# Kernel optimization log

Hardware: AMD Instinct MI355X
Metric: run time of the kernel (lower is better)

Reference implementation:

```python
import jax, jax.numpy as jnp
import numpy as np
import math

N, E, B, T = 100000, 500000, 4096, 12
IN, HID, H = 64, 32, 4
HC = HID * H  # 128
ED = 4


def setup_inputs() -> dict:
    key = jax.random.key(0)
    ks = jax.random.split(key, 40)
    w = lambda k, shape: jax.random.normal(k, shape, jnp.float32) * 0.05
    inp = {
        'x': jax.random.normal(ks[0], (N, IN), jnp.float32),
        'edge_index': jax.random.randint(ks[1], (2, E), 0, N, jnp.int32),
        'edge_attr': jax.random.normal(ks[2], (E, ED), jnp.float32),
        'batch': jnp.sort(jax.random.randint(ks[3], (N,), 0, B, jnp.int32)),
        'r_target': jax.random.randint(ks[4], (B,), 0, T, jnp.int32),
        # layer 1 (in=IN)
        'Wq1': w(ks[5], (IN, HC)), 'bq1': w(ks[6], (HC,)),
        'Wk1': w(ks[7], (IN, HC)), 'bk1': w(ks[8], (HC,)),
        'Wv1': w(ks[9], (IN, HC)), 'bv1': w(ks[10], (HC,)),
        'We1': w(ks[11], (ED, HC)),
        'Ws1': w(ks[12], (IN, HC)), 'bs1': w(ks[13], (HC,)),
        # layers 2 and 3 stacked (in=HC)
        'Wq23': w(ks[14], (2, HC, HC)), 'bq23': w(ks[15], (2, HC)),
        'Wk23': w(ks[16], (2, HC, HC)), 'bk23': w(ks[17], (2, HC)),
        'Wv23': w(ks[18], (2, HC, HC)), 'bv23': w(ks[19], (2, HC)),
        'We23': w(ks[20], (2, ED, HC)),
        'Ws23': w(ks[21], (2, HC, HC)), 'bs23': w(ks[22], (2, HC)),
        # per-task linear heads (out_channels=1)
        'head_W': w(ks[23], (T, HC)), 'head_b': w(ks[24], (T,)),
    }
    return inp


def tconv(x, src, dst, ea, Wq, bq, Wk, bk, Wv, bv, We, Ws, bs):
    """PyG TransformerConv: gather -> per-edge MHA score -> segment softmax -> scatter."""
    q = (x @ Wq + bq).reshape(-1, H, HID)   # [N,H,C]
    k = (x @ Wk + bk).reshape(-1, H, HID)
    v = (x @ Wv + bv).reshape(-1, H, HID)
    e = (ea @ We).reshape(-1, H, HID)       # [E,H,C] (lin_edge has no bias)
    kj = k[src] + e                          # [E,H,C]
    alpha = (q[dst] * kj).sum(-1) / math.sqrt(HID)          # [E,H]
    amax = jax.ops.segment_max(alpha, dst, num_segments=N)  # [N,H]
    alpha = jnp.exp(alpha - amax[dst])
    asum = jax.ops.segment_sum(alpha, dst, num_segments=N)
    alpha = alpha / (asum[dst] + 1e-16)
    msg = (v[src] + e) * alpha[..., None]                   # [E,H,C]
    out = jax.ops.segment_sum(msg, dst, num_segments=N).reshape(N, HC)
    return out + x @ Ws + bs                 # root_weight skip connection


def reference(x, edge_index, edge_attr, batch, r_target,
              Wq1, bq1, Wk1, bk1, Wv1, bv1, We1, Ws1, bs1,
              Wq23, bq23, Wk23, bk23, Wv23, bv23, We23, Ws23, bs23,
              head_W, head_b):
    src, dst = edge_index[0], edge_index[1]
    h = jax.nn.relu(tconv(x, src, dst, edge_attr, Wq1, bq1, Wk1, bk1, Wv1, bv1, We1, Ws1, bs1))
    h = jax.nn.relu(tconv(h, src, dst, edge_attr, Wq23[0], bq23[0], Wk23[0], bk23[0], Wv23[0], bv23[0], We23[0], Ws23[0], bs23[0]))
    h = tconv(h, src, dst, edge_attr, Wq23[1], bq23[1], Wk23[1], bk23[1], Wv23[1], bv23[1], We23[1], Ws23[1], bs23[1])
    # global mean pool per graph
    cnt = jax.ops.segment_sum(jnp.ones((N,), h.dtype), batch, num_segments=B)
    pooled = jax.ops.segment_sum(h, batch, num_segments=B) / jnp.maximum(cnt, 1.0)[:, None]  # [B,HC]
    # dropout p=0.3 is a no-op in eval mode
    # per-task head selected by r_target (out_channels=1, squeezed)
    return (pooled * head_W[r_target]).sum(-1) + head_b[r_target]  # [B]
```

## Files before the change

kernel.cpp:

```cpp
#include <hip/hip_runtime.h>
#include <hip/hip_bf16.h>

#define NN 100000
#define EE 500000
#define BB 4096
#define HC 128
#define SCAN_ELEM 1024
#define NSB ((NN + SCAN_ELEM - 1) / SCAN_ELEM)

typedef __bf16 bf16_t;
typedef bf16_t bf16x8 __attribute__((ext_vector_type(8)));
typedef float f32x4 __attribute__((ext_vector_type(4)));

__device__ __forceinline__ unsigned short f2bf(float f) {
    unsigned u = __builtin_bit_cast(unsigned, f);
    u += 0x7FFFu + ((u >> 16) & 1u);
    return (unsigned short)(u >> 16);
}
__device__ __forceinline__ float bflo(unsigned u) {
    return __builtin_bit_cast(float, u << 16);
}
__device__ __forceinline__ float bfhi(unsigned u) {
    return __builtin_bit_cast(float, u & 0xFFFF0000u);
}

__global__ __launch_bounds__(256) void conv_x(const float* __restrict__ in,
                                              unsigned short* __restrict__ outb,
                                              int total4)
{
    const int g = blockIdx.x * 256 + threadIdx.x;
    if (g >= total4) return;
    const float4 f = *(const float4*)(in + (size_t)g * 4);
    ushort4 u;
    u.x = f2bf(f.x); u.y = f2bf(f.y); u.z = f2bf(f.z); u.w = f2bf(f.w);
    *(ushort4*)(outb + (size_t)g * 4) = u;
}

__global__ __launch_bounds__(256) void prep_w(
    const float* __restrict__ Wq, const float* __restrict__ Wk,
    const float* __restrict__ Wv, const float* __restrict__ Ws,
    unsigned short* __restrict__ Wt, int K)
{
    const int g = blockIdx.x * 256 + threadIdx.x;
    const int per = K * 128;
    if (g >= 4 * per) return;
    const int p = g / per, r = g - p * per;
    const int k = r >> 7, n = r & 127;
    const float* W = p == 0 ? Wq : p == 1 ? Wk : p == 2 ? Wv : Ws;
    Wt[(size_t)p * per + (size_t)n * K + k] = f2bf(W[k * 128 + n]);
}

template<int NKT>
__global__ __launch_bounds__(256) void gemm_mfma(
    const unsigned short* __restrict__ A,
    const unsigned short* __restrict__ Wt,
    const float* __restrict__ bq, const float* __restrict__ bk,
    const float* __restrict__ bv, const float* __restrict__ bs,
    unsigned* __restrict__ Qb, unsigned* __restrict__ Kb,
    unsigned* __restrict__ Vb, float* __restrict__ S)
{
    constexpr int K = NKT * 32;
    const int lane = threadIdx.x & 63;
    const int p = threadIdx.x >> 6;
    const int m = lane & 15, kq = lane >> 4;
    const int rows0 = blockIdx.x * 32;

    const unsigned short* Wp = Wt + (size_t)p * 128 * K;
    const float* bias = p == 0 ? bq : p == 1 ? bk : p == 2 ? bv : bs;

    bf16x8 a[2][NKT];
#pragma unroll
    for (int mt = 0; mt < 2; mt++)
#pragma unroll
        for (int kt = 0; kt < NKT; kt++)
            a[mt][kt] = *(const bf16x8*)(A + (size_t)(rows0 + mt * 16 + m) * K + kt * 32 + kq * 8);

    f32x4 acc[2][8];
#pragma unroll
    for (int mt = 0; mt < 2; mt++)
#pragma unroll
        for (int nt = 0; nt < 8; nt++)
            acc[mt][nt] = (f32x4){0.f, 0.f, 0.f, 0.f};

#pragma unroll
    for (int nt = 0; nt < 8; nt++) {
#pragma unroll
        for (int kt = 0; kt < NKT; kt++) {
            const bf16x8 b = *(const bf16x8*)(Wp + (size_t)(nt * 16 + m) * K + kt * 32 + kq * 8);
            acc[0][nt] = __builtin_amdgcn_mfma_f32_16x16x32_bf16(a[0][kt], b, acc[0][nt], 0, 0, 0);
            acc[1][nt] = __builtin_amdgcn_mfma_f32_16x16x32_bf16(a[1][kt], b, acc[1][nt], 0, 0, 0);
        }
    }

    if (p == 3) {
#pragma unroll
        for (int nt = 0; nt < 8; nt++) {
            const float bi = bias[nt * 16 + m];
#pragma unroll
            for (int mt = 0; mt < 2; mt++) {
                float* o = S + (size_t)(rows0 + mt * 16 + kq * 4) * HC + nt * 16 + m;
#pragma unroll
                for (int r = 0; r < 4; r++) o[r * HC] = acc[mt][nt][r] + bi;
            }
        }
    } else {
        unsigned* out = p == 0 ? Qb : p == 1 ? Kb : Vb;
#pragma unroll
        for (int nt = 0; nt < 8; nt++) {
            const float bi = bias[nt * 16 + m];
#pragma unroll
            for (int mt = 0; mt < 2; mt++) {
#pragma unroll
                for (int r = 0; r < 4; r++) {
                    const float v0 = acc[mt][nt][r] + bi;
                    const float v1 = __shfl_xor(v0, 1);
                    if (!(m & 1)) {
                        const unsigned pk = (unsigned)f2bf(v0) | ((unsigned)f2bf(v1) << 16);
                        out[(size_t)(rows0 + mt * 16 + kq * 4 + r) * 64 + nt * 8 + (m >> 1)] = pk;
                    }
                }
            }
        }
    }
}

__global__ __launch_bounds__(256) void deg_k(const int* __restrict__ ei, int* __restrict__ deg)
{
    const int e = blockIdx.x * 256 + threadIdx.x;
    if (e < EE) atomicAdd(&deg[ei[EE + e]], 1);
}

__global__ __launch_bounds__(256) void scan_part(const int* __restrict__ deg,
                                                 int* __restrict__ bsum)
{
    __shared__ int red[256];
    const int base = blockIdx.x * SCAN_ELEM + threadIdx.x * 4;
    int s = 0;
#pragma unroll
    for (int j = 0; j < 4; j++) { const int i = base + j; if (i < NN) s += deg[i]; }
    red[threadIdx.x] = s;
    __syncthreads();
    for (int st = 128; st > 0; st >>= 1) {
        if (threadIdx.x < st) red[threadIdx.x] += red[threadIdx.x + st];
        __syncthreads();
    }
    if (threadIdx.x == 0) bsum[blockIdx.x] = red[0];
}

__global__ __launch_bounds__(128) void scan_top(const int* __restrict__ bsum,
                                                int* __restrict__ boff)
{
    __shared__ int buf[128];
    const int v = (threadIdx.x < NSB) ? bsum[threadIdx.x] : 0;
    buf[threadIdx.x] = v;
    __syncthreads();
    for (int s = 1; s < 128; s <<= 1) {
        const int t = (threadIdx.x >= s) ? buf[threadIdx.x - s] : 0;
        __syncthreads();
        buf[threadIdx.x] += t;
        __syncthreads();
    }
    if (threadIdx.x < NSB) boff[threadIdx.x] = buf[threadIdx.x] - v;
}

__global__ __launch_bounds__(256) void scan_final(const int* __restrict__ deg,
                                                  const int* __restrict__ boff,
                                                  int* __restrict__ off,
                                                  int* __restrict__ cursor)
{
    __shared__ int tsum[256];
    const int base = blockIdx.x * SCAN_ELEM + threadIdx.x * 4;
    int vals[4];
    int s = 0;
#pragma unroll
    for (int j = 0; j < 4; j++) {
        const int i = base + j;
        vals[j] = (i < NN) ? deg[i] : 0;
        s += vals[j];
    }
    tsum[threadIdx.x] = s;
    __syncthreads();
    for (int st = 1; st < 256; st <<= 1) {
        const int t = (threadIdx.x >= st) ? tsum[threadIdx.x - st] : 0;
        __syncthreads();
        tsum[threadIdx.x] += t;
        __syncthreads();
    }
    int ex = boff[blockIdx.x] + tsum[threadIdx.x] - s;
#pragma unroll
    for (int j = 0; j < 4; j++) {
        const int i = base + j;
        if (i < NN) { off[i] = ex; cursor[i] = ex; }
        ex += vals[j];
    }
    if (blockIdx.x == NSB - 1 && threadIdx.x == 255)
        off[NN] = boff[blockIdx.x] + tsum[255];
}

__global__ __launch_bounds__(256) void bucket_k(const int* __restrict__ ei,
                                                const float* __restrict__ ea,
                                                int* __restrict__ cursor,
                                                int* __restrict__ esrc,
                                                float4* __restrict__ eaf)
{
    const int e = blockIdx.x * 256 + threadIdx.x;
    if (e < EE) {
        const int d = ei[EE + e];
        const int p = atomicAdd(&cursor[d], 1);
        esrc[p] = ei[e];
        eaf[p] = *(const float4*)(ea + (size_t)e * 4);
    }
}

__global__ __launch_bounds__(256) void cnt_k(const int* __restrict__ batch,
                                             float* __restrict__ cnt)
{
    const int n = blockIdx.x * 256 + threadIdx.x;
    if (n < NN) atomicAdd(&cnt[batch[n]], 1.0f);
}

__global__ __launch_bounds__(256) void edge_fused(
    const int* __restrict__ esrc, const float4* __restrict__ eaf,
    const float* __restrict__ We,
    const unsigned* __restrict__ Qb, const unsigned* __restrict__ Kb,
    const unsigned* __restrict__ Vb,
    const int* __restrict__ off, const float* __restrict__ S,
    unsigned short* __restrict__ Hb,
    const int* __restrict__ batch, float* __restrict__ pooled,
    int fuse_pool)
{
    const int lane = threadIdx.x & 63;
    const int slot = lane >> 4;
    const int c8   = lane & 15;
    const int n = blockIdx.x * 4 + (threadIdx.x >> 6);

    float w[4][8];
#pragma unroll
    for (int d = 0; d < 4; d++) {
        const float4 a = *(const float4*)(We + d * HC + c8 * 8);
        const float4 b = *(const float4*)(We + d * HC + c8 * 8 + 4);
        w[d][0] = a.x; w[d][1] = a.y; w[d][2] = a.z; w[d][3] = a.w;
        w[d][4] = b.x; w[d][5] = b.y; w[d][6] = b.z; w[d][7] = b.w;
    }

    const uint4 qv = *(const uint4*)(Qb + (size_t)n * 64 + c8 * 4);
    float q[8];
    q[0] = bflo(qv.x); q[1] = bfhi(qv.x); q[2] = bflo(qv.y); q[3] = bfhi(qv.y);
    q[4] = bflo(qv.z); q[5] = bfhi(qv.z); q[6] = bflo(qv.w); q[7] = bfhi(qv.w);

    const int beg = off[n], end = off[n + 1];
    float num[8] = {0.f, 0.f, 0.f, 0.f, 0.f, 0.f, 0.f, 0.f};
    float den = 0.f;

    if (beg < end) {
        int p0 = beg + slot; if (p0 >= end) p0 = end - 1;
        int src = esrc[p0];
        float4 a4 = eaf[p0];
        for (int base = beg; base < end; base += 4) {
            const bool act = (base + slot) < end;
            const uint4 ku = *(const uint4*)(Kb + (size_t)src * 64 + c8 * 4);
            const uint4 vu = *(const uint4*)(Vb + (size_t)src * 64 + c8 * 4);
            const float4 ac = a4;
            if (base + 4 < end) {
                int pn = base + 4 + slot; if (pn >= end) pn = end - 1;
                src = esrc[pn];
                a4 = eaf[pn];
            }
            float e[8];
#pragma unroll
            for (int j = 0; j < 8; j++)
                e[j] = ac.x * w[0][j] + ac.y * w[1][j] + ac.z * w[2][j] + ac.w * w[3][j];
            float part = q[0] * (bflo(ku.x) + e[0]) + q[1] * (bfhi(ku.x) + e[1])
                       + q[2] * (bflo(ku.y) + e[2]) + q[3] * (bfhi(ku.y) + e[3])
                       + q[4] * (bflo(ku.z) + e[4]) + q[5] * (bfhi(ku.z) + e[5])
                       + q[6] * (bflo(ku.w) + e[6]) + q[7] * (bfhi(ku.w) + e[7]);
            part += __shfl_xor(part, 1);
            part += __shfl_xor(part, 2);
            float al = __expf(part * 0.17677669529663687f);
            if (!act) al = 0.f;
            num[0] += (bflo(vu.x) + e[0]) * al;
            num[1] += (bfhi(vu.x) + e[1]) * al;
            num[2] += (bflo(vu.y) + e[2]) * al;
            num[3] += (bfhi(vu.y) + e[3]) * al;
            num[4] += (bflo(vu.z) + e[4]) * al;
            num[5] += (bfhi(vu.z) + e[5]) * al;
            num[6] += (bflo(vu.w) + e[6]) * al;
            num[7] += (bfhi(vu.w) + e[7]) * al;
            den += al;
        }
    }

#pragma unroll
    for (int j = 0; j < 8; j++) {
        num[j] += __shfl_xor(num[j], 16);
        num[j] += __shfl_xor(num[j], 32);
    }
    den += __shfl_xor(den, 16);
    den += __shfl_xor(den, 32);
    const float inv = 1.f / (den + 1e-16f);

    if (!fuse_pool) {
        if (slot == 0) {
            const float4 s0 = *(const float4*)(S + (size_t)n * HC + c8 * 8);
            const float4 s1 = *(const float4*)(S + (size_t)n * HC + c8 * 8 + 4);
            float o[8];
            o[0] = fmaxf(num[0] * inv + s0.x, 0.f);
            o[1] = fmaxf(num[1] * inv + s0.y, 0.f);
            o[2] = fmaxf(num[2] * inv + s0.z, 0.f);
            o[3] = fmaxf(num[3] * inv + s0.w, 0.f);
            o[4] = fmaxf(num[4] * inv + s1.x, 0.f);
            o[5] = fmaxf(num[5] * inv + s1.y, 0.f);
            o[6] = fmaxf(num[6] * inv + s1.z, 0.f);
            o[7] = fmaxf(num[7] * inv + s1.w, 0.f);
            uint4 pk;
            pk.x = (unsigned)f2bf(o[0]) | ((unsigned)f2bf(o[1]) << 16);
            pk.y = (unsigned)f2bf(o[2]) | ((unsigned)f2bf(o[3]) << 16);
            pk.z = (unsigned)f2bf(o[4]) | ((unsigned)f2bf(o[5]) << 16);
            pk.w = (unsigned)f2bf(o[6]) | ((unsigned)f2bf(o[7]) << 16);
            *(uint4*)(Hb + (size_t)n * HC + c8 * 8) = pk;
        }
    } else {
        float oe, oo;
        if      (slot == 0) { oe = num[0]; oo = num[1]; }
        else if (slot == 1) { oe = num[2]; oo = num[3]; }
        else if (slot == 2) { oe = num[4]; oo = num[5]; }
        else                { oe = num[6]; oo = num[7]; }
        const int c = c8 * 8 + slot * 2;
        const float2 s2 = *(const float2*)(S + (size_t)n * HC + c);
        const int b = batch[n];
        atomicAdd(pooled + (size_t)b * HC + c,     oe * inv + s2.x);
        atomicAdd(pooled + (size_t)b * HC + c + 1, oo * inv + s2.y);
    }
}

__global__ __launch_bounds__(256) void head_k(
    const float* __restrict__ pooled, const float* __restrict__ cnt,
    const int* __restrict__ rt, const float* __restrict__ hW,
    const float* __restrict__ hb, float* __restrict__ out)
{
    const int lane = threadIdx.x & 63;
    const int b = blockIdx.x * 4 + (threadIdx.x >> 6);
    if (b >= BB) return;
    const int t = rt[b];
    const int c = lane * 2;
    const float2 p2 = *(const float2*)(pooled + (size_t)b * HC + c);
    const float2 w2 = *(const float2*)(hW + (size_t)t * HC + c);
    float part = p2.x * w2.x + p2.y * w2.y;
    part += __shfl_xor(part, 1);
    part += __shfl_xor(part, 2);
    part += __shfl_xor(part, 4);
    part += __shfl_xor(part, 8);
    part += __shfl_xor(part, 16);
    part += __shfl_xor(part, 32);
    if (lane == 0) out[b] = part / fmaxf(cnt[b], 1.0f) + hb[t];
}

extern "C" void kernel_launch(void* const* d_in, const int* in_sizes, int n_in,
                              void* d_out, int out_size, void* d_ws, size_t ws_size,
                              hipStream_t stream) {
    const float* x      = (const float*)d_in[0];
    const int*   ei     = (const int*)d_in[1];
    const float* ea     = (const float*)d_in[2];
    const int*   batch  = (const int*)d_in[3];
    const int*   rt     = (const int*)d_in[4];

    float* ws     = (float*)d_ws;
    float* Hbuf   = ws;
    unsigned* Qb  = (unsigned*)(ws + 12800000);
    unsigned* Kb  = Qb + 6400000;
    unsigned* Vb  = Kb + 6400000;
    unsigned short* Abf = (unsigned short*)(Vb + 6400000);
    float4* eaf   = (float4*)(Abf + 12800000);
    unsigned short* Wt = (unsigned short*)(eaf + 500000);
    float* pooled = (float*)(Wt + 65536);
    float* cnt    = pooled + 524288;
    int*   esrc   = (int*)(cnt + 4096);
    int*   deg    = esrc + 500000;
    int*   off    = deg + 100000;
    int*   cursor = off + 100004;
    int*   bsum   = cursor + 100000;
    int*   boff   = bsum + 128;

    hipMemsetAsync(deg, 0, 100000 * sizeof(int), stream);
    deg_k<<<(EE + 255) / 256, 256, 0, stream>>>(ei, deg);
    scan_part<<<NSB, 256, 0, stream>>>(deg, bsum);
    scan_top<<<1, 128, 0, stream>>>(bsum, boff);
    scan_final<<<NSB, 256, 0, stream>>>(deg, boff, off, cursor);
    bucket_k<<<(EE + 255) / 256, 256, 0, stream>>>(ei, ea, cursor, esrc, eaf);

    hipMemsetAsync(pooled, 0, (size_t)(BB * HC + BB) * sizeof(float), stream);
    cnt_k<<<(NN + 255) / 256, 256, 0, stream>>>(batch, cnt);

    conv_x<<<(NN * 64 / 4 + 255) / 256, 256, 0, stream>>>(x, Abf, NN * 64 / 4);

    for (int l = 0; l < 3; l++) {
        const int K = (l == 0) ? 64 : 128;
        const float *Wq, *Wk, *Wv, *Wsk, *bq, *bk, *bv, *bs, *We;
        if (l == 0) {
            Wq = (const float*)d_in[5];  bq = (const float*)d_in[6];
            Wk = (const float*)d_in[7];  bk = (const float*)d_in[8];
            Wv = (const float*)d_in[9];  bv = (const float*)d_in[10];
            We = (const float*)d_in[11];
            Wsk= (const float*)d_in[12]; bs = (const float*)d_in[13];
        } else {
            const int j = l - 1;
            Wq = (const float*)d_in[14] + (size_t)j * HC * HC;  bq = (const float*)d_in[15] + j * HC;
            Wk = (const float*)d_in[16] + (size_t)j * HC * HC;  bk = (const float*)d_in[17] + j * HC;
            Wv = (const float*)d_in[18] + (size_t)j * HC * HC;  bv = (const float*)d_in[19] + j * HC;
            We = (const float*)d_in[20] + (size_t)j * 4 * HC;
            Wsk= (const float*)d_in[21] + (size_t)j * HC * HC;  bs = (const float*)d_in[22] + j * HC;
        }

        prep_w<<<(4 * K * 128 + 255) / 256, 256, 0, stream>>>(Wq, Wk, Wv, Wsk, Wt, K);
        if (K == 64)
            gemm_mfma<2><<<NN / 32, 256, 0, stream>>>(Abf, Wt, bq, bk, bv, bs, Qb, Kb, Vb, Hbuf);
        else
            gemm_mfma<4><<<NN / 32, 256, 0, stream>>>(Abf, Wt, bq, bk, bv, bs, Qb, Kb, Vb, Hbuf);
        edge_fused<<<NN / 4, 256, 0, stream>>>(esrc, eaf, We, Qb, Kb, Vb, off,
                                               Hbuf, Abf, batch, pooled,
                                               l == 2 ? 1 : 0);
    }

    head_k<<<BB / 4, 256, 0, stream>>>(pooled, cnt, rt,
        (const float*)d_in[23], (const float*)d_in[24], (float*)d_out);
}
```

Before: 653.9 us.

## Factor edge-feature projection out of per-edge loop and process several nodes per wave

```diff
diff --git a/kernel.cpp b/kernel.cpp
--- a/kernel.cpp
+++ b/kernel.cpp
@@ -5,6 +5,7 @@
 #define EE 500000
 #define BB 4096
 #define HC 128
+#define NPW 8
 #define SCAN_ELEM 1024
 #define NSB ((NN + SCAN_ELEM - 1) / SCAN_ELEM)
 
@@ -229,107 +230,155 @@
     const int* __restrict__ batch, float* __restrict__ pooled,
     int fuse_pool)
 {
+    __shared__ float wes[512];
+    for (int i = threadIdx.x; i < 512; i += 256) wes[i] = We[i];
+    __syncthreads();
+
     const int lane = threadIdx.x & 63;
     const int slot = lane >> 4;
     const int c8   = lane & 15;
-    const int n = blockIdx.x * 4 + (threadIdx.x >> 6);
-
-    float w[4][8];
-#pragma unroll
-    for (int d = 0; d < 4; d++) {
-        const float4 a = *(const float4*)(We + d * HC + c8 * 8);
-        const float4 b = *(const float4*)(We + d * HC + c8 * 8 + 4);
-        w[d][0] = a.x; w[d][1] = a.y; w[d][2] = a.z; w[d][3] = a.w;
-        w[d][4] = b.x; w[d][5] = b.y; w[d][6] = b.z; w[d][7] = b.w;
-    }
-
-    const uint4 qv = *(const uint4*)(Qb + (size_t)n * 64 + c8 * 4);
-    float q[8];
-    q[0] = bflo(qv.x); q[1] = bfhi(qv.x); q[2] = bflo(qv.y); q[3] = bfhi(qv.y);
-    q[4] = bflo(qv.z); q[5] = bfhi(qv.z); q[6] = bflo(qv.w); q[7] = bfhi(qv.w);
-
-    const int beg = off[n], end = off[n + 1];
-    float num[8] = {0.f, 0.f, 0.f, 0.f, 0.f, 0.f, 0.f, 0.f};
-    float den = 0.f;
-
-    if (beg < end) {
-        int p0 = beg + slot; if (p0 >= end) p0 = end - 1;
-        int src = esrc[p0];
-        float4 a4 = eaf[p0];
+    const int cb   = c8 * 8;
+
+    int n = (blockIdx.x * 4 + (threadIdx.x >> 6)) * NPW;
+    int beg = off[n], end = off[n + 1];
+    uint4 qv = *(const uint4*)(Qb + (size_t)n * 64 + c8 * 4);
+    int src = 0;
+    float4 a4 = make_float4(0.f, 0.f, 0.f, 0.f);
+    bool pf = false;
+
+    for (int ni = 0; ni < NPW; ni++) {
+        if (!pf && beg < end) {
+            int p0 = beg + slot; if (p0 >= end) p0 = end - 1;
+            src = esrc[p0]; a4 = eaf[p0];
+        }
+        const int nn = n + 1;
+        const bool vnext = (ni + 1 < NPW);
+        int nbeg = 0, nend = 0;
+        uint4 nqv = make_uint4(0, 0, 0, 0);
+        if (vnext) {
+            nbeg = off[nn]; nend = off[nn + 1];
+            nqv = *(const uint4*)(Qb + (size_t)nn * 64 + c8 * 4);
+        }
+
+        float q[8];
+        q[0] = bflo(qv.x); q[1] = bfhi(qv.x); q[2] = bflo(qv.y); q[3] = bfhi(qv.y);
+        q[4] = bflo(qv.z); q[5] = bfhi(qv.z); q[6] = bflo(qv.w); q[7] = bfhi(qv.w);
+
+        float qe[4];
+#pragma unroll
+        for (int d = 0; d < 4; d++) {
+            const float4 wa = *(const float4*)&wes[d * HC + cb];
+            const float4 wb = *(const float4*)&wes[d * HC + cb + 4];
+            qe[d] = wa.x * q[0] + wa.y * q[1] + wa.z * q[2] + wa.w * q[3]
+                  + wb.x * q[4] + wb.y * q[5] + wb.z * q[6] + wb.w * q[7];
+            qe[d] += __shfl_xor(qe[d], 1);
+            qe[d] += __shfl_xor(qe[d], 2);
+        }
+
+        float4 sk0 = make_float4(0, 0, 0, 0), sk1 = make_float4(0, 0, 0, 0);
+        float2 sk2 = make_float2(0, 0);
+        if (!fuse_pool) {
+            if (slot == 0) {
+                sk0 = *(const float4*)(S + (size_t)n * HC + cb);
+                sk1 = *(const float4*)(S + (size_t)n * HC + cb + 4);
+            }
+        } else {
+            sk2 = *(const float2*)(S + (size_t)n * HC + cb + slot * 2);
+        }
+
+        float num[8] = {0.f, 0.f, 0.f, 0.f, 0.f, 0.f, 0.f, 0.f};
+        float s4[4] = {0.f, 0.f, 0.f, 0.f};
+        float den = 0.f;
+        bool pfn = false;
+
         for (int base = beg; base < end; base += 4) {
             const bool act = (base + slot) < end;
             const uint4 ku = *(const uint4*)(Kb + (size_t)src * 64 + c8 * 4);
             const uint4 vu = *(const uint4*)(Vb + (size_t)src * 64 + c8 * 4);
             const float4 ac = a4;
             if (base + 4 < end) {
-                int pn = base + 4 + slot; if (pn >= end) pn = end - 1;
-                src = esrc[pn];
-                a4 = eaf[pn];
+                int np = base + 4 + slot; if (np >= end) np = end - 1;
+                src = esrc[np]; a4 = eaf[np];
+            } else if (vnext && nbeg < nend) {
+                int np = nbeg + slot; if (np >= nend) np = nend - 1;
+                src = esrc[np]; a4 = eaf[np];
+                pfn = true;
             }
-            float e[8];
-#pragma unroll
-            for (int j = 0; j < 8; j++)
-                e[j] = ac.x * w[0][j] + ac.y * w[1][j] + ac.z * w[2][j] + ac.w * w[3][j];
-            float part = q[0] * (bflo(ku.x) + e[0]) + q[1] * (bfhi(ku.x) + e[1])
-                       + q[2] * (bflo(ku.y) + e[2]) + q[3] * (bfhi(ku.y) + e[3])
-                       + q[4] * (bflo(ku.z) + e[4]) + q[5] * (bfhi(ku.z) + e[5])
-                       + q[6] * (bflo(ku.w) + e[6]) + q[7] * (bfhi(ku.w) + e[7]);
+            float part = q[0] * bflo(ku.x) + q[1] * bfhi(ku.x)
+                       + q[2] * bflo(ku.y) + q[3] * bfhi(ku.y)
+                       + q[4] * bflo(ku.z) + q[5] * bfhi(ku.z)
+                       + q[6] * bflo(ku.w) + q[7] * bfhi(ku.w);
             part += __shfl_xor(part, 1);
             part += __shfl_xor(part, 2);
-            float al = __expf(part * 0.17677669529663687f);
+            const float ae = ac.x * qe[0] + ac.y * qe[1] + ac.z * qe[2] + ac.w * qe[3];
+            float al = __expf((part + ae) * 0.17677669529663687f);
             if (!act) al = 0.f;
-            num[0] += (bflo(vu.x) + e[0]) * al;
-            num[1] += (bfhi(vu.x) + e[1]) * al;
-            num[2] += (bflo(vu.y) + e[2]) * al;
-            num[3] += (bfhi(vu.y) + e[3]) * al;
-            num[4] += (bflo(vu.z) + e[4]) * al;
-            num[5] += (bfhi(vu.z) + e[5]) * al;
-            num[6] += (bflo(vu.w) + e[6]) * al;
-            num[7] += (bfhi(vu.w) + e[7]) * al;
+            num[0] += bflo(vu.x) * al;
+            num[1] += bfhi(vu.x) * al;
+            num[2] += bflo(vu.y) * al;
+            num[3] += bfhi(vu.y) * al;
+            num[4] += bflo(vu.z) * al;
+            num[5] += bfhi(vu.z) * al;
+            num[6] += bflo(vu.w) * al;
+            num[7] += bfhi(vu.w) * al;
+            s4[0] += ac.x * al; s4[1] += ac.y * al;
+            s4[2] += ac.z * al; s4[3] += ac.w * al;
             den += al;
         }
-    }
-
-#pragma unroll
-    for (int j = 0; j < 8; j++) {
-        num[j] += __shfl_xor(num[j], 16);
-        num[j] += __shfl_xor(num[j], 32);
-    }
-    den += __shfl_xor(den, 16);
-    den += __shfl_xor(den, 32);
-    const float inv = 1.f / (den + 1e-16f);
-
-    if (!fuse_pool) {
-        if (slot == 0) {
-            const float4 s0 = *(const float4*)(S + (size_t)n * HC + c8 * 8);
-            const float4 s1 = *(const float4*)(S + (size_t)n * HC + c8 * 8 + 4);
-            float o[8];
-            o[0] = fmaxf(num[0] * inv + s0.x, 0.f);
-            o[1] = fmaxf(num[1] * inv + s0.y, 0.f);
-            o[2] = fmaxf(num[2] * inv + s0.z, 0.f);
-            o[3] = fmaxf(num[3] * inv + s0.w, 0.f);
-            o[4] = fmaxf(num[4] * inv + s1.x, 0.f);
-            o[5] = fmaxf(num[5] * inv + s1.y, 0.f);
-            o[6] = fmaxf(num[6] * inv + s1.z, 0.f);
-            o[7] = fmaxf(num[7] * inv + s1.w, 0.f);
-            uint4 pk;
-            pk.x = (unsigned)f2bf(o[0]) | ((unsigned)f2bf(o[1]) << 16);
-            pk.y = (unsigned)f2bf(o[2]) | ((unsigned)f2bf(o[3]) << 16);
-            pk.z = (unsigned)f2bf(o[4]) | ((unsigned)f2bf(o[5]) << 16);
-            pk.w = (unsigned)f2bf(o[6]) | ((unsigned)f2bf(o[7]) << 16);
-            *(uint4*)(Hb + (size_t)n * HC + c8 * 8) = pk;
-        }
-    } else {
-        float oe, oo;
-        if      (slot == 0) { oe = num[0]; oo = num[1]; }
-        else if (slot == 1) { oe = num[2]; oo = num[3]; }
-        else if (slot == 2) { oe = num[4]; oo = num[5]; }
-        else                { oe = num[6]; oo = num[7]; }
-        const int c = c8 * 8 + slot * 2;
-        const float2 s2 = *(const float2*)(S + (size_t)n * HC + c);
-        const int b = batch[n];
-        atomicAdd(pooled + (size_t)b * HC + c,     oe * inv + s2.x);
-        atomicAdd(pooled + (size_t)b * HC + c + 1, oo * inv + s2.y);
+
+#pragma unroll
+        for (int j = 0; j < 8; j++) {
+            num[j] += __shfl_xor(num[j], 16);
+            num[j] += __shfl_xor(num[j], 32);
+        }
+#pragma unroll
+        for (int d = 0; d < 4; d++) {
+            s4[d] += __shfl_xor(s4[d], 16);
+            s4[d] += __shfl_xor(s4[d], 32);
+        }
+        den += __shfl_xor(den, 16);
+        den += __shfl_xor(den, 32);
+        const float inv = 1.f / (den + 1e-16f);
+
+        if (!fuse_pool) {
+            if (slot == 0) {
+                float o[8];
+#pragma unroll
+                for (int j = 0; j < 8; j++) {
+                    const float ev = s4[0] * wes[cb + j] + s4[1] * wes[HC + cb + j]
+                                   + s4[2] * wes[2 * HC + cb + j] + s4[3] * wes[3 * HC + cb + j];
+                    o[j] = (num[j] + ev) * inv;
+                }
+                o[0] = fmaxf(o[0] + sk0.x, 0.f); o[1] = fmaxf(o[1] + sk0.y, 0.f);
+                o[2] = fmaxf(o[2] + sk0.z, 0.f); o[3] = fmaxf(o[3] + sk0.w, 0.f);
+                o[4] = fmaxf(o[4] + sk1.x, 0.f); o[5] = fmaxf(o[5] + sk1.y, 0.f);
+                o[6] = fmaxf(o[6] + sk1.z, 0.f); o[7] = fmaxf(o[7] + sk1.w, 0.f);
+                uint4 pk;
+                pk.x = (unsigned)f2bf(o[0]) | ((unsigned)f2bf(o[1]) << 16);
+                pk.y = (unsigned)f2bf(o[2]) | ((unsigned)f2bf(o[3]) << 16);
+                pk.z = (unsigned)f2bf(o[4]) | ((unsigned)f2bf(o[5]) << 16);
+                pk.w = (unsigned)f2bf(o[6]) | ((unsigned)f2bf(o[7]) << 16);
+                *(uint4*)(Hb + (size_t)n * HC + cb) = pk;
+            }
+        } else {
+            float oe, oo;
+            if      (slot == 0) { oe = num[0]; oo = num[1]; }
+            else if (slot == 1) { oe = num[2]; oo = num[3]; }
+            else if (slot == 2) { oe = num[4]; oo = num[5]; }
+            else                { oe = num[6]; oo = num[7]; }
+            const int c = cb + slot * 2;
+            const float e0 = s4[0] * wes[c] + s4[1] * wes[HC + c]
+                           + s4[2] * wes[2 * HC + c] + s4[3] * wes[3 * HC + c];
+            const float e1 = s4[0] * wes[c + 1] + s4[1] * wes[HC + c + 1]
+                           + s4[2] * wes[2 * HC + c + 1] + s4[3] * wes[3 * HC + c + 1];
+            const int b = batch[n];
+            atomicAdd(pooled + (size_t)b * HC + c,     (oe + e0) * inv + sk2.x);
+            atomicAdd(pooled + (size_t)b * HC + c + 1, (oo + e1) * inv + sk2.y);
+        }
+
+        pf = pfn;
+        if (vnext) { beg = nbeg; end = nend; qv = nqv; }
+        n = nn;
     }
 }
 
@@ -416,9 +465,9 @@
             gemm_mfma<2><<<NN / 32, 256, 0, stream>>>(Abf, Wt, bq, bk, bv, bs, Qb, Kb, Vb, Hbuf);
         else
             gemm_mfma<4><<<NN / 32, 256, 0, stream>>>(Abf, Wt, bq, bk, bv, bs, Qb, Kb, Vb, Hbuf);
-        edge_fused<<<NN / 4, 256, 0, stream>>>(esrc, eaf, We, Qb, Kb, Vb, off,
-                                               Hbuf, Abf, batch, pooled,
-                                               l == 2 ? 1 : 0);
+        edge_fused<<<NN / (4 * NPW), 256, 0, stream>>>(esrc, eaf, We, Qb, Kb, Vb, off,
+                                                       Hbuf, Abf, batch, pooled,
+                                                       l == 2 ? 1 : 0);
     }
 
     head_k<<<BB / 4, 256, 0, stream>>>(pooled, cnt, rt,
```

Result: slower. 749.5 us (+14.6%).
